# Kernel tuning notes

Hardware: AMD Instinct MI355X
Metric: run time of the kernel (lower is better)

## Reference

```python
import jax, jax.numpy as jnp
import numpy as np

H_FEAT, W_FEAT, STRIDE = 75, 120, 16
IM_H, IM_W = H_FEAT * STRIDE, W_FEAT * STRIDE
NUM_ANCH = 9
PRE_NMS, POST_NMS, NMS_THRESH = 6000, 300, 0.7
CROP_SZ, POOL_SZ = 14, 7


def _generate_anchors(base_size=16, ratios=(0.5, 1.0, 2.0), scales=(8, 16, 32)):
    def whctrs(a):
        w = a[2] - a[0] + 1.0
        h = a[3] - a[1] + 1.0
        return w, h, a[0] + 0.5 * (w - 1), a[1] + 0.5 * (h - 1)

    def mk(ws, hs, xc, yc):
        ws = ws[:, None]
        hs = hs[:, None]
        return np.hstack([xc - 0.5 * (ws - 1), yc - 0.5 * (hs - 1), xc + 0.5 * (ws - 1), yc + 0.5 * (hs - 1)])

    base = np.array([0.0, 0.0, base_size - 1.0, base_size - 1.0])
    w, h, xc, yc = whctrs(base)
    size = w * h
    ws = np.round(np.sqrt(size / np.array(ratios)))
    hs = np.round(ws * np.array(ratios))
    ratio_anchors = mk(ws, hs, xc, yc)
    out = []
    for ra in ratio_anchors:
        w, h, xc, yc = whctrs(ra)
        out.append(mk(w * np.array(scales), h * np.array(scales), xc, yc))
    return np.vstack(out).astype(np.float32)


def _all_anchors():
    base = _generate_anchors()
    sx, sy = np.meshgrid(np.arange(W_FEAT) * STRIDE, np.arange(H_FEAT) * STRIDE)
    shifts = np.stack([sx.ravel(), sy.ravel(), sx.ravel(), sy.ravel()], 1).astype(np.float32)
    return (shifts[:, None, :] + base[None, :, :]).reshape(-1, 4)  # [H*W*A, 4], (h, w, a) order


_ANCHORS = jnp.asarray(_all_anchors())


def _conv(x, w, b, pad):
    y = jax.lax.conv_general_dilated(x, w, (1, 1), pad, dimension_numbers=('NCHW', 'OIHW', 'NCHW'))
    return y + b[None, :, None, None]


def _decode_clip(anchors, deltas):
    w = anchors[:, 2] - anchors[:, 0] + 1.0
    h = anchors[:, 3] - anchors[:, 1] + 1.0
    cx = anchors[:, 0] + 0.5 * w
    cy = anchors[:, 1] + 0.5 * h
    pcx = deltas[:, 0] * w + cx
    pcy = deltas[:, 1] * h + cy
    pw = jnp.exp(deltas[:, 2]) * w
    ph = jnp.exp(deltas[:, 3]) * h
    boxes = jnp.stack([pcx - 0.5 * pw, pcy - 0.5 * ph, pcx + 0.5 * pw, pcy + 0.5 * ph], 1)
    hi = jnp.array([IM_W - 1.0, IM_H - 1.0, IM_W - 1.0, IM_H - 1.0], boxes.dtype)
    return jnp.clip(boxes, 0.0, hi)


def _nms(boxes, scores, thresh, max_out):
    # boxes are sorted by score descending; classic greedy NMS with +1 area convention
    x1, y1, x2, y2 = boxes[:, 0], boxes[:, 1], boxes[:, 2], boxes[:, 3]
    areas = (x2 - x1 + 1.0) * (y2 - y1 + 1.0)
    n = boxes.shape[0]
    ar = jnp.arange(n)

    def body(i, keep):
        xx1 = jnp.maximum(x1[i], x1)
        yy1 = jnp.maximum(y1[i], y1)
        xx2 = jnp.minimum(x2[i], x2)
        yy2 = jnp.minimum(y2[i], y2)
        inter = jnp.maximum(xx2 - xx1 + 1.0, 0.0) * jnp.maximum(yy2 - yy1 + 1.0, 0.0)
        iou = inter / (areas[i] + areas - inter)
        sup = (iou > thresh) & (ar > i) & keep[i]
        return keep & (~sup)

    keep = jax.lax.fori_loop(0, n, body, jnp.ones((n,), bool))
    masked = jnp.where(keep, scores, -jnp.inf)
    _, idx = jax.lax.top_k(masked, max_out)  # preserves score order among kept boxes
    return idx


def _crop_and_resize(feat, boxes_norm, P):
    # feat: [C, Hf, Wf]; boxes_norm: [N, 4] = (y1, x1, y2, x2) normalized by (dim - 1)
    # TF crop_and_resize semantics (crop_size > 1 branch) as used by CropAndResizeFunction
    C, Hf, Wf = feat.shape
    y1, x1, y2, x2 = boxes_norm[:, 0], boxes_norm[:, 1], boxes_norm[:, 2], boxes_norm[:, 3]
    t = jnp.arange(P, dtype=feat.dtype) / (P - 1)
    ys = (y1[:, None] + t[None, :] * (y2 - y1)[:, None]) * (Hf - 1)  # [N, P]
    xs = (x1[:, None] + t[None, :] * (x2 - x1)[:, None]) * (Wf - 1)  # [N, P]
    yf = jnp.floor(ys)
    xf = jnp.floor(xs)
    wy = (ys - yf)[:, :, None]  # [N, P, 1]
    wx = (xs - xf)[:, None, :]  # [N, 1, P]
    yl = jnp.clip(yf, 0, Hf - 1).astype(jnp.int32)
    yh = jnp.clip(yl + 1, 0, Hf - 1)
    xl = jnp.clip(xf, 0, Wf - 1).astype(jnp.int32)
    xh = jnp.clip(xl + 1, 0, Wf - 1)

    def g(yi, xi):  # -> [C, N, P, P]
        return feat[:, yi[:, :, None], xi[:, None, :]]

    top = g(yl, xl) * (1 - wx) + g(yl, xh) * wx
    bot = g(yh, xl) * (1 - wx) + g(yh, xh) * wx
    out = top * (1 - wy) + bot * wy  # [C, N, P, P]
    return out.transpose(1, 0, 2, 3)  # [N, C, P, P]


def reference(net_conv, rpn_w, rpn_b, cls_w, cls_b, bbox_w, bbox_b):
    # _region_proposal: 3x3 RPN conv + ReLU, 1x1 cls / bbox heads
    rpn = jax.nn.relu(_conv(net_conv, rpn_w, rpn_b, 'SAME'))
    cls_score = _conv(rpn, cls_w, cls_b, 'VALID')   # [1, 2A, H, W]
    bbox_pred = _conv(rpn, bbox_w, bbox_b, 'VALID')  # [1, 4A, H, W]

    # softmax pairing channel a (bg) with channel A+a (fg), as in the view(1,2,-1,W) trick
    probs = jax.nn.softmax(cls_score[0].reshape(2, NUM_ANCH, H_FEAT, W_FEAT), axis=0)
    fg = probs[1].transpose(1, 2, 0).reshape(-1)              # (h, w, a) order
    deltas = bbox_pred[0].transpose(1, 2, 0).reshape(-1, 4)   # (h, w, a) order

    # proposal_layer: decode, clip, pre-NMS top-k, greedy NMS, post-NMS top-N
    proposals = _decode_clip(_ANCHORS, deltas)
    scores_k, idx = jax.lax.top_k(fg, PRE_NMS)
    boxes_k = proposals[idx]
    keep = _nms(boxes_k, scores_k, NMS_THRESH, POST_NMS)
    rois = jax.lax.stop_gradient(boxes_k[keep])  # rois.detach() in the original; [300, 4] image coords

    # _crop_pool_layer: coords / 16, normalize by (dim-1), 14x14 crop, 2x2 max pool
    fb = rois / float(STRIDE)
    bn = jnp.stack([fb[:, 1] / (H_FEAT - 1), fb[:, 0] / (W_FEAT - 1),
                    fb[:, 3] / (H_FEAT - 1), fb[:, 2] / (W_FEAT - 1)], 1)
    crops = _crop_and_resize(net_conv[0], bn, CROP_SZ)  # [300, 512, 14, 14]
    N, C = crops.shape[0], crops.shape[1]
    pooled = crops.reshape(N, C, POOL_SZ, 2, POOL_SZ, 2).max(axis=(3, 5))  # [300, 512, 7, 7]
    return pooled


def setup_inputs() -> dict:
    key = jax.random.key(0)
    ks = jax.random.split(key, 4)
    return {
        'net_conv': jax.random.normal(ks[0], (1, 512, H_FEAT, W_FEAT), jnp.float32),
        'rpn_w': jax.random.normal(ks[1], (512, 512, 3, 3), jnp.float32) * 0.01,
        'rpn_b': jnp.zeros((512,), jnp.float32),
        'cls_w': jax.random.normal(ks[2], (2 * NUM_ANCH, 512, 1, 1), jnp.float32) * 0.01,
        'cls_b': jnp.zeros((2 * NUM_ANCH,), jnp.float32),
        'bbox_w': jax.random.normal(ks[3], (4 * NUM_ANCH, 512, 1, 1), jnp.float32) * 0.01,
        'bbox_b': jnp.zeros((4 * NUM_ANCH,), jnp.float32),
    }
```

## Files before the change

kernel.cpp:

```cpp
#include <hip/hip_runtime.h>
#include <hip/hip_bf16.h>
#include <math.h>

#define HFEAT 75
#define WFEAT 120
#define NPIX (HFEAT*WFEAT)
#define NANCH 81000
#define PRE 6000
#define POST 300
#define SUPW 94
#define HBITS 18
#define HBUCK (1<<HBITS)
#define HCHUNK (HBUCK/1024)

typedef __attribute__((ext_vector_type(4))) float f32x4;
typedef __attribute__((ext_vector_type(8))) short short8;

__constant__ float ANCH[9][4] = {
  {-84.f,-40.f,99.f,55.f},  {-176.f,-88.f,191.f,103.f},{-360.f,-184.f,375.f,199.f},
  {-56.f,-56.f,71.f,71.f},  {-120.f,-120.f,135.f,135.f},{-248.f,-248.f,263.f,263.f},
  {-36.f,-80.f,51.f,95.f},  {-80.f,-168.f,95.f,183.f}, {-168.f,-344.f,183.f,359.f}};

__device__ inline void split3(float a, short& s1, short& s2, short& s3) {
  __hip_bfloat16 b1 = __float2bfloat16(a);
  float r = a - __bfloat162float(b1);
  __hip_bfloat16 b2 = __float2bfloat16(r);
  float r2 = r - __bfloat162float(b2);
  __hip_bfloat16 b3 = __float2bfloat16(r2);
  s1 = __builtin_bit_cast(short, b1);
  s2 = __builtin_bit_cast(short, b2);
  s3 = __builtin_bit_cast(short, b3);
}

__global__ void wtrans(const float* __restrict__ w, float* __restrict__ wt) {
  int i = blockIdx.x * 256 + threadIdx.x;
  if (i >= 9 * 512 * 512) return;
  int t = i / (512 * 512);
  int r = i - t * 512 * 512;
  int oc = r >> 9, ic = r & 511;
  wt[i] = w[(size_t)oc * 4608 + ic * 9 + t];
}

__global__ __launch_bounds__(256) void conv3_mfma(
    const float* __restrict__ in, const float* __restrict__ wt,
    const float* __restrict__ bias, float* __restrict__ out)
{
  __shared__ __align__(16) short in_b[3][3][66][40];
  const int tid = threadIdx.x;
  const int lane = tid & 63, wv = tid >> 6;
  const int wm = wv >> 1, wn = wv & 1;
  const int fr = lane & 15, fq = lane >> 4;
  const int y = blockIdx.x;
  const int x0 = blockIdx.y * 56;
  const int ocb = blockIdx.z * 64;
  const int ko = fq * 8;

  f32x4 acc[2][2] = {};

  const float* wrow0 = wt + (size_t)(ocb + wn * 32 + 0 * 16 + fr) * 512 + ko;
  const float* wrow1 = wt + (size_t)(ocb + wn * 32 + 1 * 16 + fr) * 512 + ko;

  f32x4 bw[2][2], bwN[2][2];
  bw[0][0] = *(const f32x4*)(wrow0);      bw[0][1] = *(const f32x4*)(wrow0 + 4);
  bw[1][0] = *(const f32x4*)(wrow1);      bw[1][1] = *(const f32x4*)(wrow1 + 4);

  for (int c0 = 0; c0 < 512; c0 += 32) {
    __syncthreads();
    for (int u = tid; u < 792; u += 256) {
      int dy = u / 264; int r = u - dy * 264;
      int icg = r / 66; int cc = r - icg * 66;
      int gy = y + dy - 1, gx = x0 - 1 + cc;
      bool ok = ((unsigned)gy < 75u) && ((unsigned)gx < 120u);
      const float* ip = in + (size_t)(c0 + icg * 8) * NPIX + gy * WFEAT + gx;
      short8 v1, v2, v3;
      #pragma unroll
      for (int j = 0; j < 8; ++j) {
        float v = ok ? ip[j * NPIX] : 0.f;
        short a, b, c; split3(v, a, b, c);
        v1[j] = a; v2[j] = b; v3[j] = c;
      }
      *(short8*)&in_b[0][dy][cc][icg * 8] = v1;
      *(short8*)&in_b[1][dy][cc][icg * 8] = v2;
      *(short8*)&in_b[2][dy][cc][icg * 8] = v3;
    }
    __syncthreads();

    for (int t = 0; t < 9; ++t) {
      short8 bfrag[3][2];
      #pragma unroll
      for (int n = 0; n < 2; ++n) {
        float tmp[8] = {bw[n][0].x, bw[n][0].y, bw[n][0].z, bw[n][0].w,
                        bw[n][1].x, bw[n][1].y, bw[n][1].z, bw[n][1].w};
        #pragma unroll
        for (int j = 0; j < 8; ++j) {
          short a, b, c; split3(tmp[j], a, b, c);
          bfrag[0][n][j] = a; bfrag[1][n][j] = b; bfrag[2][n][j] = c;
        }
      }
      {
        int nt = t + 1, nc = c0;
        if (nt == 9) { nt = 0; nc += 32; }
        if (nc < 512) {
          const float* p0 = wrow0 + (size_t)nt * 262144 + nc;
          const float* p1 = wrow1 + (size_t)nt * 262144 + nc;
          bwN[0][0] = *(const f32x4*)p0; bwN[0][1] = *(const f32x4*)(p0 + 4);
          bwN[1][0] = *(const f32x4*)p1; bwN[1][1] = *(const f32x4*)(p1 + 4);
        }
      }
      const int dy = t / 3, dx = t - dy * 3;
      short8 af[3][2];
      #pragma unroll
      for (int m = 0; m < 2; ++m) {
        int col = wm * 32 + m * 16 + fr + dx;
        #pragma unroll
        for (int s = 0; s < 3; ++s)
          af[s][m] = *(const short8*)&in_b[s][dy][col][ko];
      }
      const int pa[6] = {2, 0, 1, 1, 0, 0};
      const int pb[6] = {0, 2, 1, 0, 1, 0};
      #pragma unroll
      for (int p = 0; p < 6; ++p)
        #pragma unroll
        for (int m = 0; m < 2; ++m)
          #pragma unroll
          for (int n = 0; n < 2; ++n)
            acc[m][n] = __builtin_amdgcn_mfma_f32_16x16x32_bf16(
                af[pa[p]][m], bfrag[pb[p]][n], acc[m][n], 0, 0, 0);
      bw[0][0] = bwN[0][0]; bw[0][1] = bwN[0][1];
      bw[1][0] = bwN[1][0]; bw[1][1] = bwN[1][1];
    }
  }

  #pragma unroll
  for (int n = 0; n < 2; ++n) {
    int oc = ocb + wn * 32 + n * 16 + fr;
    float bv = bias[oc];
    #pragma unroll
    for (int m = 0; m < 2; ++m) {
      #pragma unroll
      for (int r = 0; r < 4; ++r) {
        int px = wm * 32 + m * 16 + fq * 4 + r;
        float v = acc[m][n][r] + bv;
        out[(size_t)oc * NPIX + y * WFEAT + x0 + px] = v > 0.f ? v : 0.f;
      }
    }
  }
}

__global__ __launch_bounds__(256) void conv1x1(
    const float* __restrict__ rpn,
    const float* __restrict__ wc, const float* __restrict__ bc,
    const float* __restrict__ wb, const float* __restrict__ bb,
    float* __restrict__ cls, float* __restrict__ bbox)
{
  __shared__ float r_s[64][128];
  __shared__ float w_s[54][64];
  const int tid = threadIdx.x;
  const int px0 = blockIdx.x * 128;
  const int px = tid & 127, g = tid >> 7;
  float tot[27];
  #pragma unroll
  for (int j = 0; j < 27; ++j) tot[j] = 0.f;
  for (int ic0 = 0; ic0 < 512; ic0 += 64) {
    __syncthreads();
    for (int i = tid; i < 64*128; i += 256) {
      int ic = i >> 7, p = i & 127;
      int gp = px0 + p;
      r_s[ic][p] = (gp < NPIX) ? rpn[(ic0 + ic) * NPIX + gp] : 0.f;
    }
    for (int i = tid; i < 54*64; i += 256) {
      int c = i >> 6, ic = i & 63;
      w_s[c][ic] = (c < 18) ? wc[c * 512 + ic0 + ic] : wb[(c - 18) * 512 + ic0 + ic];
    }
    __syncthreads();
    float acc[27];
    #pragma unroll
    for (int j = 0; j < 27; ++j) acc[j] = 0.f;
    for (int ic = 0; ic < 64; ++ic) {
      float iv = r_s[ic][px];
      #pragma unroll
      for (int j = 0; j < 27; ++j) acc[j] += iv * w_s[g * 27 + j][ic];
    }
    #pragma unroll
    for (int j = 0; j < 27; ++j) tot[j] += acc[j];
  }
  int gp = px0 + px;
  if (gp < NPIX) {
    for (int j = 0; j < 27; ++j) {
      int c = g * 27 + j;
      if (c < 18) cls[c * NPIX + gp] = tot[j] + bc[c];
      else        bbox[(c - 18) * NPIX + gp] = tot[j] + bb[c - 18];
    }
  }
}

__device__ inline unsigned long long dkey(double d) {
  long long b = __double_as_longlong(d);
  unsigned long long u = (unsigned long long)b;
  return (b < 0) ? ~u : (u | 0x8000000000000000ull);
}

__global__ void decode_score(
    const float* __restrict__ cls, const float* __restrict__ bbox,
    float* __restrict__ props, unsigned long long* __restrict__ keys)
{
  int i = blockIdx.x * 256 + threadIdx.x;
  if (i >= NANCH) return;
  int a = i % 9, p = i / 9;
  int x = p % WFEAT, y = p / WFEAT;
  float c0 = cls[a * NPIX + p], c1 = cls[(9 + a) * NPIX + p];
  double d = (double)c1 - (double)c0;
  unsigned long long s = dkey(d);
  keys[i] = (s & ~0x1FFFFull) | (unsigned long long)(0x1FFFFu - (unsigned)i);

  double ax1 = (double)ANCH[a][0] + 16.0 * x;
  double ay1 = (double)ANCH[a][1] + 16.0 * y;
  double ax2 = (double)ANCH[a][2] + 16.0 * x;
  double ay2 = (double)ANCH[a][3] + 16.0 * y;
  double aw = ax2 - ax1 + 1.0, ah = ay2 - ay1 + 1.0;
  double cx = ax1 + 0.5 * aw,  cy = ay1 + 0.5 * ah;
  double d0 = (double)bbox[(4*a+0) * NPIX + p];
  double d1 = (double)bbox[(4*a+1) * NPIX + p];
  double d2 = (double)bbox[(4*a+2) * NPIX + p];
  double d3 = (double)bbox[(4*a+3) * NPIX + p];
  double pcx = d0 * aw + cx, pcy = d1 * ah + cy;
  double pw = exp(d2) * aw,  ph = exp(d3) * ah;
  double bx1 = pcx - 0.5 * pw, by1 = pcy - 0.5 * ph;
  double bx2 = pcx + 0.5 * pw, by2 = pcy + 0.5 * ph;
  bx1 = fmin(fmax(bx1, 0.0), 1919.0); by1 = fmin(fmax(by1, 0.0), 1199.0);
  bx2 = fmin(fmax(bx2, 0.0), 1919.0); by2 = fmin(fmax(by2, 0.0), 1199.0);
  props[i*4+0] = (float)bx1; props[i*4+1] = (float)by1;
  props[i*4+2] = (float)bx2; props[i*4+3] = (float)by2;
}

__global__ void hist_hi(const unsigned long long* __restrict__ keys,
                        unsigned* __restrict__ hist)
{
  int i = blockIdx.x * 256 + threadIdx.x;
  if (i < NANCH) atomicAdd(&hist[(unsigned)(keys[i] >> 46)], 1u);
}

__global__ __launch_bounds__(1024) void select_thresh(
    const unsigned long long* __restrict__ keys,
    const unsigned* __restrict__ hist, unsigned long long* __restrict__ thresh)
{
  __shared__ unsigned csum[1024];
  __shared__ int sh_bucket, sh_rank, sh_cnt;
  __shared__ unsigned long long buf[4096];
  const int tid = threadIdx.x;
  unsigned s = 0;
  for (int i = 0; i < HCHUNK; ++i) s += hist[tid * HCHUNK + i];
  csum[tid] = s;
  __syncthreads();
  if (tid == 0) {
    unsigned cum = 0; int tc = 0;
    for (int t = 1023; t >= 0; --t) {
      if (cum + csum[t] >= PRE) { tc = t; break; }
      cum += csum[t];
    }
    int B = tc * HCHUNK;
    for (int b0 = HCHUNK - 1; b0 >= 0; --b0) {
      unsigned h = hist[tc * HCHUNK + b0];
      if (cum + h >= PRE) { B = tc * HCHUNK + b0; break; }
      cum += h;
    }
    sh_bucket = B;
    sh_rank = PRE - (int)cum;
    sh_cnt = 0;
  }
  __syncthreads();
  const int B = sh_bucket, r = sh_rank;
  for (int i = tid; i < NANCH; i += 1024) {
    unsigned long long kv = keys[i];
    if ((int)(kv >> 46) == B) {
      int p = atomicAdd(&sh_cnt, 1);
      if (p < 4096) buf[p] = kv;
    }
  }
  __syncthreads();
  int c = sh_cnt < 4096 ? sh_cnt : 4096;
  for (int i = tid; i < c; i += 1024) {
    unsigned long long kv = buf[i];
    int gt = 0;
    for (int j = 0; j < c; ++j) gt += (buf[j] > kv) ? 1 : 0;
    if (gt == r - 1) *thresh = kv;
  }
}

__global__ void compact_ge(const unsigned long long* __restrict__ keys,
                           const unsigned long long* __restrict__ thresh,
                           unsigned long long* __restrict__ keys2,
                           unsigned* __restrict__ counter)
{
  int i = blockIdx.x * 256 + threadIdx.x;
  if (i >= NANCH) return;
  unsigned long long kv = keys[i];
  if (kv >= *thresh) keys2[atomicAdd(counter, 1u)] = kv;
}

__global__ __launch_bounds__(1024) void sort8192(unsigned long long* __restrict__ keys2)
{
  extern __shared__ unsigned long long s[];
  const int tid = threadIdx.x;
  for (int e = tid; e < 8192; e += 1024) s[e] = (e < PRE) ? keys2[e] : 0ull;
  __syncthreads();
  for (int k = 2; k <= 8192; k <<= 1) {
    for (int j = k >> 1; j >= 1; j >>= 1) {
      for (int e = tid; e < 4096; e += 1024) {
        int lo = ((e & ~(j - 1)) << 1) | (e & (j - 1));
        int hi = lo + j;
        bool dirDesc = ((lo & k) == 0);
        unsigned long long a = s[lo], b = s[hi];
        if (dirDesc ? (a < b) : (a > b)) { s[lo] = b; s[hi] = a; }
      }
      __syncthreads();
    }
  }
  for (int e = tid; e < PRE; e += 1024) keys2[e] = s[e];
}

__global__ void gather_topk(const unsigned long long* __restrict__ keys2,
                            const float* __restrict__ props, float* __restrict__ boxes)
{
  int i = blockIdx.x * 256 + threadIdx.x;
  if (i >= PRE) return;
  unsigned idx = 0x1FFFFu - (unsigned)(keys2[i] & 0x1FFFFull);
  ((float4*)boxes)[i] = ((const float4*)props)[idx];
}

__global__ __launch_bounds__(64) void nms_sup(const float* __restrict__ boxes,
                                              unsigned long long* __restrict__ sup)
{
  const int bi = blockIdx.x, bj = blockIdx.y;
  const int j0 = bj * 64;
  __shared__ float4 cb[64];
  int jt = j0 + threadIdx.x;
  cb[threadIdx.x] = (jt < PRE) ? ((const float4*)boxes)[jt] : make_float4(0,0,0,0);
  __syncthreads();
  int i = bi * 64 + threadIdx.x;
  if (i >= PRE) return;
  float4 b = ((const float4*)boxes)[i];
  double x1 = b.x, y1 = b.y, x2 = b.z, y2 = b.w;
  double area_i = (x2 - x1 + 1.0) * (y2 - y1 + 1.0);
  unsigned long long m = 0ull;
  for (int jj = 0; jj < 64; ++jj) {
    int j = j0 + jj;
    if (j > i && j < PRE) {
      float4 c = cb[jj];
      double xx1 = fmax(x1, (double)c.x), yy1 = fmax(y1, (double)c.y);
      double xx2 = fmin(x2, (double)c.z), yy2 = fmin(y2, (double)c.w);
      double iw = xx2 - xx1 + 1.0, ih = yy2 - yy1 + 1.0;
      if (iw > 0.0 && ih > 0.0) {
        double inter = iw * ih;
        double area_j = ((double)c.z - c.x + 1.0) * ((double)c.w - c.y + 1.0);
        double iou = inter / (area_i + area_j - inter);
        if (iou > 0.7) m |= (1ull << jj);
      }
    }
  }
  sup[(long)i * SUPW + bj] = m;
}

__global__ __launch_bounds__(64) void nms_scan(const unsigned long long* __restrict__ sup,
                                               const float* __restrict__ boxes,
                                               float* __restrict__ rois)
{
  __shared__ unsigned long long keep[SUPW];
  __shared__ unsigned long long supl[64];
  __shared__ int kpre[SUPW], spre[SUPW];
  __shared__ int totK;
  __shared__ int pos[POST];
  const int tid = threadIdx.x;
  for (int w = tid; w < SUPW; w += 64) keep[w] = ~0ull;
  __syncthreads();

  for (int b = 0; b < SUPW; ++b) {
    int i = b * 64 + tid;
    supl[tid] = (i < PRE) ? sup[(long)i * SUPW + b] : 0ull;
    __syncthreads();
    unsigned long long kw = keep[b];
    #pragma unroll 8
    for (int k = 0; k < 64; ++k)
      kw &= ~(supl[k] & (0ull - ((kw >> k) & 1ull)));
    if (tid == 0) keep[b] = kw;
    const unsigned long long* colbase = sup + (long)(b * 64) * SUPW;
    for (int wdx = b + 1 + tid; wdx < SUPW; wdx += 64) {
      unsigned long long acc = 0ull;
      #pragma unroll 8
      for (int k = 0; k < 64; ++k)
        acc |= colbase[(long)k * SUPW + wdx] & (0ull - ((kw >> k) & 1ull));
      keep[wdx] &= ~acc;
    }
    __syncthreads();
  }

  if (tid == 0) {
    int kc = 0, sc = 0;
    for (int w = 0; w < SUPW; ++w) {
      unsigned long long valid = (w == SUPW - 1) ? ((1ull << 48) - 1ull) : ~0ull;
      kpre[w] = kc; spre[w] = sc;
      kc += __popcll(keep[w] & valid);
      sc += __popcll(~keep[w] & valid);
    }
    totK = kc;
  }
  __syncthreads();
  const int K = totK;
  for (int w = tid; w < SUPW; w += 64) {
    unsigned long long valid = (w == SUPW - 1) ? ((1ull << 48) - 1ull) : ~0ull;
    unsigned long long kk = keep[w] & valid;
    int r = kpre[w];
    while (kk && r < POST) {
      int k_ = __builtin_ctzll(kk); kk &= kk - 1ull;
      pos[r++] = w * 64 + k_;
    }
    unsigned long long ss = ~keep[w] & valid;
    int r2 = K + spre[w];
    while (ss && r2 < POST) {
      int k_ = __builtin_ctzll(ss); ss &= ss - 1ull;
      pos[r2++] = w * 64 + k_;
    }
  }
  __syncthreads();
  for (int t = tid; t < POST * 4; t += 64)
    rois[t] = boxes[pos[t >> 2] * 4 + (t & 3)];
}

__global__ __launch_bounds__(256) void crop_pool(
    const float* __restrict__ feat, const float* __restrict__ rois,
    float* __restrict__ out)
{
  __shared__ int xl[14], xh[14], yl[14], yh[14];
  __shared__ float wx[14], wy[14];
  const int n = blockIdx.x;
  const int tid = threadIdx.x;
  if (tid < 14) {
    float4 r = ((const float4*)rois)[n];
    double fx1 = (double)r.x / 16.0, fy1 = (double)r.y / 16.0;
    double fx2 = (double)r.z / 16.0, fy2 = (double)r.w / 16.0;
    double x1n = fx1 / 119.0, x2n = fx2 / 119.0;
    double y1n = fy1 / 74.0,  y2n = fy2 / 74.0;
    double t = (double)tid / 13.0;
    double xs = (x1n + t * (x2n - x1n)) * 119.0;
    double ys = (y1n + t * (y2n - y1n)) * 74.0;
    double xf = floor(xs), yf = floor(ys);
    wx[tid] = (float)(xs - xf);
    wy[tid] = (float)(ys - yf);
    int xli = (int)fmin(fmax(xf, 0.0), 119.0);
    int yli = (int)fmin(fmax(yf, 0.0), 74.0);
    xl[tid] = xli; xh[tid] = (xli + 1 > 119) ? 119 : xli + 1;
    yl[tid] = yli; yh[tid] = (yli + 1 > 74) ? 74 : yli + 1;
  }
  __syncthreads();
  for (int t = tid; t < 512 * 49; t += 256) {
    int c = t / 49, r = t % 49;
    int py = r / 7, px = r % 7;
    const float* fc = feat + c * NPIX;
    float m = -1e30f;
    #pragma unroll
    for (int sy = 0; sy < 2; ++sy) {
      int iy = py * 2 + sy;
      float wyv = wy[iy];
      int ylo = yl[iy] * WFEAT, yhi = yh[iy] * WFEAT;
      #pragma unroll
      for (int sx = 0; sx < 2; ++sx) {
        int ix = px * 2 + sx;
        float wxv = wx[ix];
        float v00 = fc[ylo + xl[ix]], v01 = fc[ylo + xh[ix]];
        float v10 = fc[yhi + xl[ix]], v11 = fc[yhi + xh[ix]];
        float top = v00 * (1.f - wxv) + v01 * wxv;
        float bot = v10 * (1.f - wxv) + v11 * wxv;
        float val = top * (1.f - wyv) + bot * wyv;
        m = fmaxf(m, val);
      }
    }
    out[(n * 512 + c) * 49 + r] = m;
  }
}

extern "C" void kernel_launch(void* const* d_in, const int* in_sizes, int n_in,
                              void* d_out, int out_size, void* d_ws, size_t ws_size,
                              hipStream_t stream) {
  const float* net    = (const float*)d_in[0];
  const float* rpn_w  = (const float*)d_in[1];
  const float* rpn_b  = (const float*)d_in[2];
  const float* cls_w  = (const float*)d_in[3];
  const float* cls_b  = (const float*)d_in[4];
  const float* bbox_w = (const float*)d_in[5];
  const float* bbox_b = (const float*)d_in[6];
  float* out = (float*)d_out;

  float* rpn = out;
  unsigned* hist = (unsigned*)(out + 4608000);
  unsigned* counter = hist + HBUCK;
  unsigned long long* thresh = (unsigned long long*)(counter + 2);
  unsigned long long* keys2 = thresh + 1;
  float* wt = (float*)(keys2 + PRE);

  float* cls   = (float*)d_ws;
  float* bbox  = cls + 162000;
  float* props = bbox + 324000;
  unsigned long long* keys = (unsigned long long*)(props + 324000);
  float* boxes_k = (float*)(keys + 131072);
  unsigned long long* sup = (unsigned long long*)(boxes_k + PRE * 4);
  float* rois = (float*)(sup + (size_t)PRE * SUPW);

  wtrans<<<(9 * 512 * 512 + 255) / 256, 256, 0, stream>>>(rpn_w, wt);
  conv3_mfma<<<dim3(75, 2, 8), 256, 0, stream>>>(net, wt, rpn_b, rpn);
  conv1x1<<<71, 256, 0, stream>>>(rpn, cls_w, cls_b, bbox_w, bbox_b, cls, bbox);
  decode_score<<<(NANCH + 255) / 256, 256, 0, stream>>>(cls, bbox, props, keys);

  hipMemsetAsync(hist, 0, (size_t)(HBUCK + 1) * 4, stream);
  hist_hi<<<(NANCH + 255) / 256, 256, 0, stream>>>(keys, hist);
  select_thresh<<<1, 1024, 0, stream>>>(keys, hist, thresh);
  compact_ge<<<(NANCH + 255) / 256, 256, 0, stream>>>(keys, thresh, keys2, counter);
  sort8192<<<1, 1024, 65536, stream>>>(keys2);
  gather_topk<<<(PRE + 255) / 256, 256, 0, stream>>>(keys2, props, boxes_k);

  dim3 gsup(SUPW, SUPW);
  nms_sup<<<gsup, 64, 0, stream>>>(boxes_k, sup);
  nms_scan<<<1, 64, 0, stream>>>(sup, boxes_k, rois);
  crop_pool<<<POST, 256, 0, stream>>>(net, rois, out);
}
```

Before: 1.628 ms.

## Transpose NMS suppression matrix and widen serial scan to 256 threads

The suppression bitmask matrix is stored column-block-major (block index outer, box index inner), so the serial NMS scan can read each 64-word column chunk contiguously with 16-byte vector loads instead of strided loads. The scan kernel goes from 64 to 256 threads so all remaining word columns are covered in one pass per block rather than looping. This targets the latency-bound single-block scan; the nms_sup writes become coalesced too. It costs more idle threads per step.

New measurement: 1.498 ms. 1.09x faster.

```diff
diff --git a/kernel.cpp b/kernel.cpp
--- a/kernel.cpp
+++ b/kernel.cpp
@@ -329,7 +329,7 @@
 }
 
 __global__ __launch_bounds__(64) void nms_sup(const float* __restrict__ boxes,
-                                              unsigned long long* __restrict__ sup)
+                                              unsigned long long* __restrict__ supT)
 {
   const int bi = blockIdx.x, bj = blockIdx.y;
   const int j0 = bj * 64;
@@ -358,12 +358,12 @@
       }
     }
   }
-  sup[(long)i * SUPW + bj] = m;
-}
-
-__global__ __launch_bounds__(64) void nms_scan(const unsigned long long* __restrict__ sup,
-                                               const float* __restrict__ boxes,
-                                               float* __restrict__ rois)
+  supT[(size_t)bj * PRE + i] = m;
+}
+
+__global__ __launch_bounds__(256) void nms_scan(const unsigned long long* __restrict__ supT,
+                                                const float* __restrict__ boxes,
+                                                float* __restrict__ rois)
 {
   __shared__ unsigned long long keep[SUPW];
   __shared__ unsigned long long supl[64];
@@ -371,24 +371,31 @@
   __shared__ int totK;
   __shared__ int pos[POST];
   const int tid = threadIdx.x;
-  for (int w = tid; w < SUPW; w += 64) keep[w] = ~0ull;
+  for (int w = tid; w < SUPW; w += 256) keep[w] = ~0ull;
   __syncthreads();
 
   for (int b = 0; b < SUPW; ++b) {
-    int i = b * 64 + tid;
-    supl[tid] = (i < PRE) ? sup[(long)i * SUPW + b] : 0ull;
+    unsigned long long kw = keep[b];
+    if (tid < 64) {
+      int i = b * 64 + tid;
+      supl[tid] = (i < PRE) ? supT[(size_t)b * PRE + i] : 0ull;
+    }
     __syncthreads();
-    unsigned long long kw = keep[b];
     #pragma unroll 8
     for (int k = 0; k < 64; ++k)
       kw &= ~(supl[k] & (0ull - ((kw >> k) & 1ull)));
     if (tid == 0) keep[b] = kw;
-    const unsigned long long* colbase = sup + (long)(b * 64) * SUPW;
-    for (int wdx = b + 1 + tid; wdx < SUPW; wdx += 64) {
+    int wdx = b + 1 + tid;
+    if (wdx < SUPW) {
+      const ulonglong2* p =
+          (const ulonglong2*)(supT + (size_t)wdx * PRE + b * 64);
       unsigned long long acc = 0ull;
       #pragma unroll 8
-      for (int k = 0; k < 64; ++k)
-        acc |= colbase[(long)k * SUPW + wdx] & (0ull - ((kw >> k) & 1ull));
+      for (int q = 0; q < 32; ++q) {
+        ulonglong2 v = p[q];
+        acc |= v.x & (0ull - ((kw >> (2 * q)) & 1ull));
+        acc |= v.y & (0ull - ((kw >> (2 * q + 1)) & 1ull));
+      }
       keep[wdx] &= ~acc;
     }
     __syncthreads();
@@ -406,7 +413,7 @@
   }
   __syncthreads();
   const int K = totK;
-  for (int w = tid; w < SUPW; w += 64) {
+  for (int w = tid; w < SUPW; w += 256) {
     unsigned long long valid = (w == SUPW - 1) ? ((1ull << 48) - 1ull) : ~0ull;
     unsigned long long kk = keep[w] & valid;
     int r = kpre[w];
@@ -422,7 +429,7 @@
     }
   }
   __syncthreads();
-  for (int t = tid; t < POST * 4; t += 64)
+  for (int t = tid; t < POST * 4; t += 256)
     rois[t] = boxes[pos[t >> 2] * 4 + (t & 3)];
 }
 
@@ -502,8 +509,8 @@
   float* props = bbox + 324000;
   unsigned long long* keys = (unsigned long long*)(props + 324000);
   float* boxes_k = (float*)(keys + 131072);
-  unsigned long long* sup = (unsigned long long*)(boxes_k + PRE * 4);
-  float* rois = (float*)(sup + (size_t)PRE * SUPW);
+  unsigned long long* supT = (unsigned long long*)(boxes_k + PRE * 4);
+  float* rois = (float*)(supT + (size_t)SUPW * PRE);
 
   wtrans<<<(9 * 512 * 512 + 255) / 256, 256, 0, stream>>>(rpn_w, wt);
   conv3_mfma<<<dim3(75, 2, 8), 256, 0, stream>>>(net, wt, rpn_b, rpn);
@@ -518,7 +525,7 @@
   gather_topk<<<(PRE + 255) / 256, 256, 0, stream>>>(keys2, props, boxes_k);
 
   dim3 gsup(SUPW, SUPW);
-  nms_sup<<<gsup, 64, 0, stream>>>(boxes_k, sup);
-  nms_scan<<<1, 64, 0, stream>>>(sup, boxes_k, rois);
+  nms_sup<<<gsup, 64, 0, stream>>>(boxes_k, supT);
+  nms_scan<<<1, 256, 0, stream>>>(supT, boxes_k, rois);
   crop_pool<<<POST, 256, 0, stream>>>(net, rois, out);
 }
```
